# Kernel tuning notes

Measured on AMD Instinct MI355X. Metric: run time of the kernel, lower is better.

## Reference

```python
import jax, jax.numpy as jnp
import numpy as np

NUM_CHEM = 60000
NUM_DIS = 40000
N = NUM_CHEM + NUM_DIS  # 100000 nodes
H = 128                 # hidden_dim
L = 2                   # num_layers
E = 800000              # number of CD training pairs (directed edges = 2*E)
B = 65536               # number of query pairs


def setup_inputs() -> dict:
    key = jax.random.key(0)
    ks = jax.random.split(key, 9)
    scale = 1.0 / np.sqrt(H)
    node_emb = jax.random.normal(ks[0], (N, H), jnp.float32) * 0.02
    Wrel = jax.random.normal(ks[1], (L, 2, H, H), jnp.float32) * scale
    Wroot = jax.random.normal(ks[2], (L, H, H), jnp.float32) * scale
    bias = jnp.zeros((L, H), jnp.float32)
    Wscore = jax.random.normal(ks[3], (H, H), jnp.float32) * scale
    # replicate _build_cd_bipartite_buffers: forward edges (rel 0) then reverse (rel 1)
    chem_e = jax.random.randint(ks[4], (E,), 0, NUM_CHEM)
    dis_e = jax.random.randint(ks[5], (E,), 0, NUM_DIS) + NUM_CHEM
    src = jnp.concatenate([chem_e, dis_e])  # [2E]
    dst = jnp.concatenate([dis_e, chem_e])  # [2E]
    chem_ids = jax.random.randint(ks[6], (B,), 0, NUM_CHEM)
    dis_ids = jax.random.randint(ks[7], (B,), 0, NUM_DIS)
    return {"node_emb": node_emb, "Wrel": Wrel, "Wroot": Wroot, "bias": bias,
            "Wscore": Wscore, "src": src, "dst": dst,
            "chem_ids": chem_ids, "dis_ids": dis_ids}


def _mean_agg(msg, dst_idx, dtype):
    # scatter-mean: sum messages per destination node, divide by edge count
    s = jax.ops.segment_sum(msg, dst_idx, num_segments=N)            # [N,H]
    cnt = jax.ops.segment_sum(jnp.ones(msg.shape[0], dtype), dst_idx, num_segments=N)
    return s / jnp.maximum(cnt, 1.0)[:, None]


def _rgcn_layer(x, src, dst, Wr, Wroot_l, b):
    # edges statically ordered: first E are relation 0, last E relation 1
    src0, src1 = src[:E], src[E:]
    dst0, dst1 = dst[:E], dst[E:]
    agg0 = _mean_agg(x[src0] @ Wr[0], dst0, x.dtype)  # gather -> transform -> scatter-mean
    agg1 = _mean_agg(x[src1] @ Wr[1], dst1, x.dtype)
    return x @ Wroot_l + b + agg0 + agg1


def reference(node_emb, Wrel, Wroot, bias, Wscore, src, dst, chem_ids, dis_ids):
    x = node_emb
    for l in range(L):
        x = _rgcn_layer(x, src, dst, Wrel[l], Wroot[l], bias[l])
        if l + 1 < L:
            x = jax.nn.relu(x)  # dropout p=0.0 (eval) is identity
    zc, zd = x[:NUM_CHEM], x[NUM_CHEM:]
    c = zc[chem_ids]  # [B,H]
    d = zd[dis_ids]   # [B,H]
    return jnp.sum((c @ Wscore) * d, axis=-1)  # bilinear pair score [B]
```

## Files before the change

kernel.cpp:

```cpp
#include <hip/hip_runtime.h>
#include <hip/hip_bf16.h>

#define NUM_CHEM 60000
#define NUM_DIS  40000
#define NN       100000
#define HD       128
#define E1       800000
#define E2       1600000
#define NB       65536
#define SCAN_B   391
#define CHEM_TB  469
#define DIS_TB   313

typedef __attribute__((ext_vector_type(8))) short short8;
typedef __attribute__((ext_vector_type(4))) float f32x4;

__device__ __forceinline__ unsigned short f2bf(float f) {
    unsigned u = __builtin_bit_cast(unsigned, f);
    u = (u + 0x7fffu + ((u >> 16) & 1u)) >> 16;
    return (unsigned short)u;
}
__device__ __forceinline__ float bf2f(short h) {
    unsigned u = ((unsigned)(unsigned short)h) << 16;
    return __builtin_bit_cast(float, u);
}
__device__ __forceinline__ short8 ldfrag(const short* p) {
    return *reinterpret_cast<const short8*>(p);
}

__global__ void degcount_k(const int* __restrict__ dst, int* __restrict__ deg) {
    int e = blockIdx.x * blockDim.x + threadIdx.x;
    if (e < E2) atomicAdd(&deg[dst[e]], 1);
}

__global__ void scan1_k(const int* __restrict__ deg, int* __restrict__ row,
                        int* __restrict__ bsum) {
    __shared__ int s[256];
    int tid = threadIdx.x;
    int g = blockIdx.x * 256 + tid;
    int v = (g < NN) ? deg[g] : 0;
    s[tid] = v;
    __syncthreads();
    for (int off = 1; off < 256; off <<= 1) {
        int t = (tid >= off) ? s[tid - off] : 0;
        __syncthreads();
        s[tid] += t;
        __syncthreads();
    }
    if (g < NN) row[g] = s[tid] - v;
    if (tid == 255) bsum[blockIdx.x] = s[255];
}

__global__ void scan2_k(int* __restrict__ bsum) {
    __shared__ int s[512];
    int tid = threadIdx.x;
    int v = (tid < SCAN_B) ? bsum[tid] : 0;
    s[tid] = v;
    __syncthreads();
    for (int off = 1; off < 512; off <<= 1) {
        int t = (tid >= off) ? s[tid - off] : 0;
        __syncthreads();
        s[tid] += t;
        __syncthreads();
    }
    if (tid < SCAN_B) bsum[tid] = s[tid] - v;
}

__global__ void scan3_k(int* __restrict__ row, const int* __restrict__ bsum) {
    int g = blockIdx.x * 256 + threadIdx.x;
    if (g < NN) row[g] += bsum[blockIdx.x];
}

__global__ void fill_k(const int* __restrict__ src, const int* __restrict__ dst,
                       const int* __restrict__ row, int* __restrict__ cursor,
                       int* __restrict__ csr) {
    int e = blockIdx.x * blockDim.x + threadIdx.x;
    if (e >= E2) return;
    int d = dst[e];
    int p = atomicAdd(&cursor[d], 1);
    csr[row[d] + p] = src[e];
}

__global__ void cvt_k(const float* __restrict__ src, short* __restrict__ dst) {
    int i = blockIdx.x * 256 + threadIdx.x;
    if (i >= NN * HD / 8) return;
    const float4* s4 = (const float4*)src;
    float4 a = s4[2 * i], b = s4[2 * i + 1];
    short8 o;
    o[0] = (short)f2bf(a.x); o[1] = (short)f2bf(a.y);
    o[2] = (short)f2bf(a.z); o[3] = (short)f2bf(a.w);
    o[4] = (short)f2bf(b.x); o[5] = (short)f2bf(b.y);
    o[6] = (short)f2bf(b.z); o[7] = (short)f2bf(b.w);
    ((short8*)dst)[i] = o;
}

__global__ void wprep_k(const float* __restrict__ Wrel, const float* __restrict__ Wroot,
                        const float* __restrict__ Wscore, short* __restrict__ WT) {
    int m = blockIdx.x;
    const float* src;
    switch (m) {
        case 0: src = Wroot; break;
        case 1: src = Wrel; break;
        case 2: src = Wrel + 16384; break;
        case 3: src = Wroot + 16384; break;
        case 4: src = Wrel + 2 * 16384; break;
        case 5: src = Wrel + 3 * 16384; break;
        default: src = Wscore; break;
    }
    short* dstm = WT + m * 16384;
    for (int i = threadIdx.x; i < 16384; i += 256) {
        int k = i >> 7, n = i & 127;
        dstm[n * 128 + k] = (short)f2bf(src[i]);
    }
}

__global__ void gather_k(const int* __restrict__ csr, const int* __restrict__ rowp,
                         const int* __restrict__ deg, const short* __restrict__ x,
                         short* __restrict__ agg) {
    int t = blockIdx.x * 256 + threadIdx.x;
    int n = t >> 4;
    if (n >= NN) return;
    int f = (t & 15) * 8;
    int base = rowp[n], d = deg[n];
    float a[8];
#pragma unroll
    for (int i = 0; i < 8; ++i) a[i] = 0.f;
    int j = 0;
    for (; j + 1 < d; j += 2) {
        int s0 = csr[base + j], s1 = csr[base + j + 1];
        short8 u = ldfrag(x + (size_t)s0 * HD + f);
        short8 v = ldfrag(x + (size_t)s1 * HD + f);
#pragma unroll
        for (int i = 0; i < 8; ++i) a[i] += bf2f(u[i]) + bf2f(v[i]);
    }
    if (j < d) {
        int s0 = csr[base + j];
        short8 u = ldfrag(x + (size_t)s0 * HD + f);
#pragma unroll
        for (int i = 0; i < 8; ++i) a[i] += bf2f(u[i]);
    }
    float sc = 1.0f / fmaxf((float)d, 1.0f);
    short8 o;
#pragma unroll
    for (int i = 0; i < 8; ++i) o[i] = (short)f2bf(a[i] * sc);
    *(short8*)(agg + (size_t)n * HD + f) = o;
}

__global__ __launch_bounds__(256)
void transform_k(const short* __restrict__ x, short* __restrict__ agg,
                 const short* __restrict__ WrootT, const short* __restrict__ WrelT,
                 const float* __restrict__ bias_l, int do_relu) {
    int b = blockIdx.x;
    int base, limit;
    const short* WrT;
    if (b < CHEM_TB) { base = b * 128; limit = NUM_CHEM; WrT = WrelT + 16384; }
    else { base = NUM_CHEM + (b - CHEM_TB) * 128; limit = NN; WrT = WrelT; }
    int lane = threadIdx.x & 63, w = threadIdx.x >> 6;
    int l15 = lane & 15, lg = lane >> 4;
    int rb = base + w * 32;
    int m0 = rb + l15, m1 = m0 + 16;
    bool v0 = m0 < limit, v1 = m1 < limit;
    f32x4 acc[2][8];
#pragma unroll
    for (int mt = 0; mt < 2; ++mt)
#pragma unroll
        for (int nt = 0; nt < 8; ++nt) acc[mt][nt] = (f32x4){0.f, 0.f, 0.f, 0.f};
    const short8 zero8 = (short8){0, 0, 0, 0, 0, 0, 0, 0};
#pragma unroll
    for (int ks = 0; ks < 4; ++ks) {
        int ko = ks * 32 + lg * 8;
        short8 ax0 = v0 ? ldfrag(x + (size_t)m0 * HD + ko) : zero8;
        short8 ax1 = v1 ? ldfrag(x + (size_t)m1 * HD + ko) : zero8;
        short8 ag0 = v0 ? ldfrag(agg + (size_t)m0 * HD + ko) : zero8;
        short8 ag1 = v1 ? ldfrag(agg + (size_t)m1 * HD + ko) : zero8;
#pragma unroll
        for (int nt = 0; nt < 8; ++nt) {
            short8 br = ldfrag(WrootT + (nt * 16 + l15) * HD + ko);
            short8 bg = ldfrag(WrT + (nt * 16 + l15) * HD + ko);
            acc[0][nt] = __builtin_amdgcn_mfma_f32_16x16x32_bf16(ax0, br, acc[0][nt], 0, 0, 0);
            acc[1][nt] = __builtin_amdgcn_mfma_f32_16x16x32_bf16(ax1, br, acc[1][nt], 0, 0, 0);
            acc[0][nt] = __builtin_amdgcn_mfma_f32_16x16x32_bf16(ag0, bg, acc[0][nt], 0, 0, 0);
            acc[1][nt] = __builtin_amdgcn_mfma_f32_16x16x32_bf16(ag1, bg, acc[1][nt], 0, 0, 0);
        }
    }
#pragma unroll
    for (int mt = 0; mt < 2; ++mt) {
#pragma unroll
        for (int r = 0; r < 4; ++r) {
            int row = rb + mt * 16 + lg * 4 + r;
            if (row < limit) {
#pragma unroll
                for (int nt = 0; nt < 8; ++nt) {
                    int col = nt * 16 + l15;
                    float v = acc[mt][nt][r] + bias_l[col];
                    if (do_relu) v = fmaxf(v, 0.f);
                    agg[(size_t)row * HD + col] = (short)f2bf(v);
                }
            }
        }
    }
}

__global__ __launch_bounds__(256)
void scoregemm_k(const short* __restrict__ x, const short* __restrict__ WT,
                 short* __restrict__ zcp) {
    int base = blockIdx.x * 128;
    int lane = threadIdx.x & 63, w = threadIdx.x >> 6;
    int l15 = lane & 15, lg = lane >> 4;
    int rb = base + w * 32;
    int m0 = rb + l15, m1 = m0 + 16;
    bool v0 = m0 < NUM_CHEM, v1 = m1 < NUM_CHEM;
    f32x4 acc[2][8];
#pragma unroll
    for (int mt = 0; mt < 2; ++mt)
#pragma unroll
        for (int nt = 0; nt < 8; ++nt) acc[mt][nt] = (f32x4){0.f, 0.f, 0.f, 0.f};
    const short8 zero8 = (short8){0, 0, 0, 0, 0, 0, 0, 0};
#pragma unroll
    for (int ks = 0; ks < 4; ++ks) {
        int ko = ks * 32 + lg * 8;
        short8 a0 = v0 ? ldfrag(x + (size_t)m0 * HD + ko) : zero8;
        short8 a1 = v1 ? ldfrag(x + (size_t)m1 * HD + ko) : zero8;
#pragma unroll
        for (int nt = 0; nt < 8; ++nt) {
            short8 bw = ldfrag(WT + (nt * 16 + l15) * HD + ko);
            acc[0][nt] = __builtin_amdgcn_mfma_f32_16x16x32_bf16(a0, bw, acc[0][nt], 0, 0, 0);
            acc[1][nt] = __builtin_amdgcn_mfma_f32_16x16x32_bf16(a1, bw, acc[1][nt], 0, 0, 0);
        }
    }
#pragma unroll
    for (int mt = 0; mt < 2; ++mt) {
#pragma unroll
        for (int r = 0; r < 4; ++r) {
            int row = rb + mt * 16 + lg * 4 + r;
            if (row < NUM_CHEM) {
#pragma unroll
                for (int nt = 0; nt < 8; ++nt) {
                    int col = nt * 16 + l15;
                    zcp[(size_t)row * HD + col] = (short)f2bf(acc[mt][nt][r]);
                }
            }
        }
    }
}

__global__ void dot_k(const short* __restrict__ zcp, const short* __restrict__ xfin,
                      const int* __restrict__ chem_ids, const int* __restrict__ dis_ids,
                      float* __restrict__ out) {
    int t = blockIdx.x * 256 + threadIdx.x;
    int p = t >> 4;
    if (p >= NB) return;
    int f = (t & 15) * 8;
    int c = chem_ids[p];
    int dn = NUM_CHEM + dis_ids[p];
    short8 a = ldfrag(zcp + (size_t)c * HD + f);
    short8 b = ldfrag(xfin + (size_t)dn * HD + f);
    float s = 0.f;
#pragma unroll
    for (int i = 0; i < 8; ++i) s += bf2f(a[i]) * bf2f(b[i]);
    s += __shfl_xor(s, 1);
    s += __shfl_xor(s, 2);
    s += __shfl_xor(s, 4);
    s += __shfl_xor(s, 8);
    if ((t & 15) == 0) out[p] = s;
}

extern "C" void kernel_launch(void* const* d_in, const int* in_sizes, int n_in,
                              void* d_out, int out_size, void* d_ws, size_t ws_size,
                              hipStream_t stream) {
    const float* node_emb = (const float*)d_in[0];
    const float* Wrel     = (const float*)d_in[1];
    const float* Wroot    = (const float*)d_in[2];
    const float* bias     = (const float*)d_in[3];
    const float* Wscore   = (const float*)d_in[4];
    const int*   src      = (const int*)d_in[5];
    const int*   dst      = (const int*)d_in[6];
    const int*   chem_ids = (const int*)d_in[7];
    const int*   dis_ids  = (const int*)d_in[8];
    float* out = (float*)d_out;

    const size_t XB = (size_t)NN * HD * 2;
    const size_t ZB = (size_t)NUM_CHEM * HD * 2;
    char* ws = (char*)d_ws;
    short* P    = (short*)(ws);
    short* Q    = (short*)(ws + XB);
    short* R    = (short*)(ws + 2 * XB);
    short* WT   = (short*)(ws + 2 * XB + ZB);
    char*  ip   = ws + 2 * XB + ZB + 7 * 16384 * 2;
    int* deg    = (int*)(ip);
    int* rowp   = (int*)(ip + 400000);
    int* cursor = (int*)(ip + 800000);
    int* bsum   = (int*)(ip + 1200000);
    int* csr    = (int*)(ip + 1204096);

    hipMemsetAsync(deg, 0, NN * sizeof(int), stream);
    hipMemsetAsync(cursor, 0, NN * sizeof(int), stream);
    degcount_k<<<(E2 + 255) / 256, 256, 0, stream>>>(dst, deg);
    scan1_k<<<SCAN_B, 256, 0, stream>>>(deg, rowp, bsum);
    scan2_k<<<1, 512, 0, stream>>>(bsum);
    scan3_k<<<SCAN_B, 256, 0, stream>>>(rowp, bsum);
    fill_k<<<(E2 + 255) / 256, 256, 0, stream>>>(src, dst, rowp, cursor, csr);

    cvt_k<<<(NN * HD / 8 + 255) / 256, 256, 0, stream>>>(node_emb, P);
    wprep_k<<<7, 256, 0, stream>>>(Wrel, Wroot, Wscore, WT);

    gather_k<<<(NN * 16 + 255) / 256, 256, 0, stream>>>(csr, rowp, deg, P, Q);
    transform_k<<<CHEM_TB + DIS_TB, 256, 0, stream>>>(P, Q, WT, WT + 16384, bias, 1);

    gather_k<<<(NN * 16 + 255) / 256, 256, 0, stream>>>(csr, rowp, deg, Q, P);
    transform_k<<<CHEM_TB + DIS_TB, 256, 0, stream>>>(Q, P, WT + 3 * 16384,
                                                      WT + 4 * 16384, bias + HD, 0);

    scoregemm_k<<<CHEM_TB, 256, 0, stream>>>(P, WT + 6 * 16384, R);
    dot_k<<<NB * 16 / 256, 256, 0, stream>>>(R, P, chem_ids, dis_ids, out);
}
```

Baseline: 516.4 us.

## Fuse neighbor gather into layer GEMM via LDS and compress CSR indices

Each layer's mean-aggregation gather now runs inside the transform kernel. Aggregated rows go into a swizzled shared-memory tile instead of a global buffer, which removes one global write and read of the aggregate per layer and two kernel launches. CSR source indices are stored as 16-bit offsets relative to the chem or disease partition. The cursor array is seeded from the prefix scan, which drops a memset and the row lookup in the fill kernel. The trade-offs: 32KB of LDS per block may lower occupancy, and the gather work per block is less balanced than in a standalone gather kernel.

```diff
diff --git a/kernel.cpp b/kernel.cpp
--- a/kernel.cpp
+++ b/kernel.cpp
@@ -66,19 +66,24 @@
     if (tid < SCAN_B) bsum[tid] = s[tid] - v;
 }
 
-__global__ void scan3_k(int* __restrict__ row, const int* __restrict__ bsum) {
+__global__ void scan3_k(int* __restrict__ row, int* __restrict__ cursor,
+                        const int* __restrict__ bsum) {
     int g = blockIdx.x * 256 + threadIdx.x;
-    if (g < NN) row[g] += bsum[blockIdx.x];
+    if (g < NN) {
+        int v = row[g] + bsum[blockIdx.x];
+        row[g] = v;
+        cursor[g] = v;
+    }
 }
 
 __global__ void fill_k(const int* __restrict__ src, const int* __restrict__ dst,
-                       const int* __restrict__ row, int* __restrict__ cursor,
-                       int* __restrict__ csr) {
+                       int* __restrict__ cursor, unsigned short* __restrict__ csr16) {
     int e = blockIdx.x * blockDim.x + threadIdx.x;
     if (e >= E2) return;
     int d = dst[e];
+    int s = src[e];
     int p = atomicAdd(&cursor[d], 1);
-    csr[row[d] + p] = src[e];
+    csr16[p] = (unsigned short)(d < NUM_CHEM ? s - NUM_CHEM : s);
 }
 
 __global__ void cvt_k(const float* __restrict__ src, short* __restrict__ dst) {
@@ -114,51 +119,65 @@
     }
 }
 
-__global__ void gather_k(const int* __restrict__ csr, const int* __restrict__ rowp,
-                         const int* __restrict__ deg, const short* __restrict__ x,
-                         short* __restrict__ agg) {
-    int t = blockIdx.x * 256 + threadIdx.x;
-    int n = t >> 4;
-    if (n >= NN) return;
-    int f = (t & 15) * 8;
-    int base = rowp[n], d = deg[n];
-    float a[8];
-#pragma unroll
-    for (int i = 0; i < 8; ++i) a[i] = 0.f;
-    int j = 0;
-    for (; j + 1 < d; j += 2) {
-        int s0 = csr[base + j], s1 = csr[base + j + 1];
-        short8 u = ldfrag(x + (size_t)s0 * HD + f);
-        short8 v = ldfrag(x + (size_t)s1 * HD + f);
-#pragma unroll
-        for (int i = 0; i < 8; ++i) a[i] += bf2f(u[i]) + bf2f(v[i]);
-    }
-    if (j < d) {
-        int s0 = csr[base + j];
-        short8 u = ldfrag(x + (size_t)s0 * HD + f);
-#pragma unroll
-        for (int i = 0; i < 8; ++i) a[i] += bf2f(u[i]);
-    }
-    float sc = 1.0f / fmaxf((float)d, 1.0f);
-    short8 o;
-#pragma unroll
-    for (int i = 0; i < 8; ++i) o[i] = (short)f2bf(a[i] * sc);
-    *(short8*)(agg + (size_t)n * HD + f) = o;
-}
-
 __global__ __launch_bounds__(256)
-void transform_k(const short* __restrict__ x, short* __restrict__ agg,
-                 const short* __restrict__ WrootT, const short* __restrict__ WrelT,
-                 const float* __restrict__ bias_l, int do_relu) {
+void layer_k(const short* __restrict__ x, short* __restrict__ y,
+             const unsigned short* __restrict__ csr16, const int* __restrict__ rowp,
+             const int* __restrict__ deg,
+             const short* __restrict__ WrootT, const short* __restrict__ WrelT01,
+             const float* __restrict__ bias_l, int do_relu) {
+    __shared__ short at[128 * HD];
     int b = blockIdx.x;
-    int base, limit;
+    int base, limit, srcoff;
     const short* WrT;
-    if (b < CHEM_TB) { base = b * 128; limit = NUM_CHEM; WrT = WrelT + 16384; }
-    else { base = NUM_CHEM + (b - CHEM_TB) * 128; limit = NN; WrT = WrelT; }
-    int lane = threadIdx.x & 63, w = threadIdx.x >> 6;
+    if (b < CHEM_TB) {
+        base = b * 128; limit = NUM_CHEM; WrT = WrelT01 + 16384; srcoff = NUM_CHEM;
+    } else {
+        base = NUM_CHEM + (b - CHEM_TB) * 128; limit = NN; WrT = WrelT01; srcoff = 0;
+    }
+    int tid = threadIdx.x;
+
+    {
+        int grp = tid >> 4, f = tid & 15;
+        for (int rr = 0; rr < 8; ++rr) {
+            int r = rr * 16 + grp;
+            int n = base + r;
+            float a[8];
+#pragma unroll
+            for (int i = 0; i < 8; ++i) a[i] = 0.f;
+            if (n < limit) {
+                int cb = rowp[n], d = deg[n];
+                int j = 0;
+                for (; j + 1 < d; j += 2) {
+                    int s0 = csr16[cb + j] + srcoff;
+                    int s1 = csr16[cb + j + 1] + srcoff;
+                    short8 u = ldfrag(x + (size_t)s0 * HD + f * 8);
+                    short8 v = ldfrag(x + (size_t)s1 * HD + f * 8);
+#pragma unroll
+                    for (int i = 0; i < 8; ++i) a[i] += bf2f(u[i]) + bf2f(v[i]);
+                }
+                if (j < d) {
+                    int s0 = csr16[cb + j] + srcoff;
+                    short8 u = ldfrag(x + (size_t)s0 * HD + f * 8);
+#pragma unroll
+                    for (int i = 0; i < 8; ++i) a[i] += bf2f(u[i]);
+                }
+                float sc = 1.0f / fmaxf((float)d, 1.0f);
+#pragma unroll
+                for (int i = 0; i < 8; ++i) a[i] *= sc;
+            }
+            short8 o;
+#pragma unroll
+            for (int i = 0; i < 8; ++i) o[i] = (short)f2bf(a[i]);
+            int gsw = f ^ (r & 7);
+            *(short8*)&at[r * HD + gsw * 8] = o;
+        }
+    }
+    __syncthreads();
+
+    int lane = tid & 63, w = tid >> 6;
     int l15 = lane & 15, lg = lane >> 4;
-    int rb = base + w * 32;
-    int m0 = rb + l15, m1 = m0 + 16;
+    int lr0 = w * 32 + l15, lr1 = lr0 + 16;
+    int m0 = base + lr0, m1 = base + lr1;
     bool v0 = m0 < limit, v1 = m1 < limit;
     f32x4 acc[2][8];
 #pragma unroll
@@ -169,10 +188,11 @@
 #pragma unroll
     for (int ks = 0; ks < 4; ++ks) {
         int ko = ks * 32 + lg * 8;
+        int g = ks * 4 + lg;
         short8 ax0 = v0 ? ldfrag(x + (size_t)m0 * HD + ko) : zero8;
         short8 ax1 = v1 ? ldfrag(x + (size_t)m1 * HD + ko) : zero8;
-        short8 ag0 = v0 ? ldfrag(agg + (size_t)m0 * HD + ko) : zero8;
-        short8 ag1 = v1 ? ldfrag(agg + (size_t)m1 * HD + ko) : zero8;
+        short8 ag0 = *(const short8*)&at[lr0 * HD + (g ^ (lr0 & 7)) * 8];
+        short8 ag1 = *(const short8*)&at[lr1 * HD + (g ^ (lr1 & 7)) * 8];
 #pragma unroll
         for (int nt = 0; nt < 8; ++nt) {
             short8 br = ldfrag(WrootT + (nt * 16 + l15) * HD + ko);
@@ -187,14 +207,14 @@
     for (int mt = 0; mt < 2; ++mt) {
 #pragma unroll
         for (int r = 0; r < 4; ++r) {
-            int row = rb + mt * 16 + lg * 4 + r;
+            int row = base + w * 32 + mt * 16 + lg * 4 + r;
             if (row < limit) {
 #pragma unroll
                 for (int nt = 0; nt < 8; ++nt) {
                     int col = nt * 16 + l15;
                     float v = acc[mt][nt][r] + bias_l[col];
                     if (do_relu) v = fmaxf(v, 0.f);
-                    agg[(size_t)row * HD + col] = (short)f2bf(v);
+                    y[(size_t)row * HD + col] = (short)f2bf(v);
                 }
             }
         }
@@ -291,25 +311,23 @@
     int* rowp   = (int*)(ip + 400000);
     int* cursor = (int*)(ip + 800000);
     int* bsum   = (int*)(ip + 1200000);
-    int* csr    = (int*)(ip + 1204096);
+    unsigned short* csr16 = (unsigned short*)(ip + 1204096);
 
     hipMemsetAsync(deg, 0, NN * sizeof(int), stream);
-    hipMemsetAsync(cursor, 0, NN * sizeof(int), stream);
     degcount_k<<<(E2 + 255) / 256, 256, 0, stream>>>(dst, deg);
     scan1_k<<<SCAN_B, 256, 0, stream>>>(deg, rowp, bsum);
     scan2_k<<<1, 512, 0, stream>>>(bsum);
-    scan3_k<<<SCAN_B, 256, 0, stream>>>(rowp, bsum);
-    fill_k<<<(E2 + 255) / 256, 256, 0, stream>>>(src, dst, rowp, cursor, csr);
+    scan3_k<<<SCAN_B, 256, 0, stream>>>(rowp, cursor, bsum);
+    fill_k<<<(E2 + 255) / 256, 256, 0, stream>>>(src, dst, cursor, csr16);
 
     cvt_k<<<(NN * HD / 8 + 255) / 256, 256, 0, stream>>>(node_emb, P);
     wprep_k<<<7, 256, 0, stream>>>(Wrel, Wroot, Wscore, WT);
 
-    gather_k<<<(NN * 16 + 255) / 256, 256, 0, stream>>>(csr, rowp, deg, P, Q);
-    transform_k<<<CHEM_TB + DIS_TB, 256, 0, stream>>>(P, Q, WT, WT + 16384, bias, 1);
-
-    gather_k<<<(NN * 16 + 255) / 256, 256, 0, stream>>>(csr, rowp, deg, Q, P);
-    transform_k<<<CHEM_TB + DIS_TB, 256, 0, stream>>>(Q, P, WT + 3 * 16384,
-                                                      WT + 4 * 16384, bias + HD, 0);
+    layer_k<<<CHEM_TB + DIS_TB, 256, 0, stream>>>(P, Q, csr16, rowp, deg,
+                                                  WT, WT + 16384, bias, 1);
+    layer_k<<<CHEM_TB + DIS_TB, 256, 0, stream>>>(Q, P, csr16, rowp, deg,
+                                                  WT + 3 * 16384, WT + 4 * 16384,
+                                                  bias + HD, 0);
 
     scoregemm_k<<<CHEM_TB, 256, 0, stream>>>(P, WT + 6 * 16384, R);
     dot_k<<<NB * 16 / 256, 256, 0, stream>>>(R, P, chem_ids, dis_ids, out);
```

New measurement: 630.2 us. 1.22x slower.
